# Optimization experiments

Measured on AMD Instinct MI355X. Metric: run time of the kernel, lower is better.

Reference implementation:

```python
import jax, jax.numpy as jnp
import numpy as np

HEADS = 16
GN_EPS = 1e-5
NEG = -1e30  # finite stand-in for -inf to keep softmax/vjp NaN-free


def setup_inputs() -> dict:
    key = jax.random.key(0)
    k0, k1, k2, k3 = jax.random.split(key, 4)
    B, C, T = 8, 1024, 1024
    x = jax.random.normal(k0, (B, C, T), dtype=jnp.float32)
    mask = jax.random.randint(k1, (B, T), 0, 2).astype(bool)  # True = masked position
    w_kvq = jax.random.normal(k2, (3 * C, C), dtype=jnp.float32) * 0.02  # Conv1d k=1 == per-time GEMM
    w_out = jax.random.normal(k3, (C, C), dtype=jnp.float32) * 0.02
    gn_weight = jnp.ones((C,), dtype=jnp.float32)
    gn_bias = jnp.zeros((C,), dtype=jnp.float32)
    return {"x": x, "mask": mask, "w_kvq": w_kvq, "w_out": w_out,
            "gn_weight": gn_weight, "gn_bias": gn_bias}


def reference(x, mask, w_kvq, w_out, gn_weight, gn_bias):
    B, C, T = x.shape
    H = HEADS
    d = C // H
    # QKV projection (1x1 conv == GEMM over channels)
    kvq = jnp.einsum('oc,bct->bot', w_kvq, x)  # [B, 3C, T]
    k = kvq[:, :C].reshape(B, H, d, T)
    v = kvq[:, C:2 * C].reshape(B, H, d, T)
    q = kvq[:, 2 * C:].reshape(B, H, d, T)
    scale = 1.0 / np.sqrt(d).astype(np.float32)
    # att[b,h,k,q] = <k_k, q_q> / sqrt(d)
    att = jnp.einsum('bhdk,bhdq->bhkq', k, q) * scale
    # mask key rows, softmax over key axis, then zero masked query columns
    att = jnp.where(mask[:, None, :, None], NEG, att)
    att = jax.nn.softmax(att, axis=2)
    att = jnp.where(mask[:, None, None, :], 0.0, att)
    ctx = jnp.einsum('bhdk,bhkq->bhdq', v, att).reshape(B, C, T)
    out = jnp.einsum('oc,bct->bot', w_out, ctx)
    y = out + x  # residual
    # GroupNorm(1, C): normalize over (C, T) per sample, per-channel affine
    mean = jnp.mean(y, axis=(1, 2), keepdims=True)
    var = jnp.var(y, axis=(1, 2), keepdims=True)
    y = (y - mean) * jax.lax.rsqrt(var + GN_EPS)
    y = y * gn_weight[None, :, None] + gn_bias[None, :, None]
    # torch layout of returned attention: chunks over heads concatenated on batch dim
    att_ret = att.transpose(1, 0, 2, 3).reshape(H * B, T, T)
    return y, att_ret
```

## Files before the change

kernel.cpp:

```cpp
#include <hip/hip_runtime.h>

#define DEVI __device__ __forceinline__

typedef __attribute__((ext_vector_type(8))) short s16x8;
typedef __attribute__((ext_vector_type(4))) float f32x4;
typedef __attribute__((ext_vector_type(4))) unsigned short u16x4;
typedef __attribute__((ext_vector_type(4))) int i32x4;

static constexpr int NB = 8;
static constexpr int NC = 1024;
static constexpr int NT = 1024;
static constexpr int NH = 16;
static constexpr int ND = 64;

DEVI unsigned short cvt_bf16(float f) {
  unsigned int u = __builtin_bit_cast(unsigned int, f);
  u += 0x7fffu + ((u >> 16) & 1u);
  return (unsigned short)(u >> 16);
}

DEVI float fexp2(float x) {
#if __has_builtin(__builtin_amdgcn_exp2f)
  return __builtin_amdgcn_exp2f(x);
#else
  return exp2f(x);
#endif
}

template<int ROWS>
DEVI void stage_tile(const unsigned short* g, int ld, char* lds, int loff, int tid) {
  const int wave = tid >> 6;
  const int lane = tid & 63;
#pragma unroll
  for (int r = 0; r < (ROWS >> 5); ++r) {
    const int row = r * 32 + wave * 8 + (lane >> 3);
    const int c  = lane & 7;
    const int cg = c ^ (row & 7);
    const char* src = (const char*)g + (size_t)row * ld * 2 + cg * 16;
    char* dst = lds + loff + (r * 32 + wave * 8) * 128;
    __builtin_amdgcn_global_load_lds((const __attribute__((address_space(1))) void*)src,
                                     (__attribute__((address_space(3))) void*)dst,
                                     16, 0, 0);
  }
}

DEVI void stage_v(const unsigned short* v, int k0, char* lds, int loff, int tid) {
  const int wave = tid >> 6;
  const int lane = tid & 63;
#pragma unroll
  for (int it = 0; it < 4; ++it) {
    const int d = wave * 16 + it * 4 + (lane >> 4);
    const int c = lane & 15;
    const int cg = c ^ (d & 15);
    const char* src = (const char*)(v + (size_t)d * NT + k0 + cg * 8);
    char* dst = lds + loff + (wave * 16 + it * 4) * 256;
    __builtin_amdgcn_global_load_lds((const __attribute__((address_space(1))) void*)src,
                                     (__attribute__((address_space(3))) void*)dst,
                                     16, 0, 0);
  }
}

DEVI s16x8 frag_ld(const char* lds, int loff, int row, int ks, int lane) {
  const int chunk = (ks * 4 + (lane >> 4)) ^ (row & 7);
  return *(const s16x8*)(lds + loff + row * 128 + chunk * 16);
}

template<int KTOT>
DEVI void gemm_core_128(const unsigned short* A, const unsigned short* Bt,
                        int ldA, int ldB, char* lds, int tid, f32x4 acc[4][4]) {
  const int lane = tid & 63;
  const int wave = tid >> 6;
  const int wr = wave >> 1, wc = wave & 1;
#pragma unroll
  for (int i = 0; i < 4; ++i)
#pragma unroll
    for (int j = 0; j < 4; ++j)
      acc[i][j] = (f32x4){0.f, 0.f, 0.f, 0.f};
  for (int k0 = 0; k0 < KTOT; k0 += 64) {
    __syncthreads();
    stage_tile<128>(A + k0, ldA, lds, 0, tid);
    stage_tile<128>(Bt + k0, ldB, lds, 16384, tid);
    asm volatile("s_waitcnt vmcnt(0)" ::: "memory");
    __syncthreads();
#pragma unroll
    for (int ks = 0; ks < 2; ++ks) {
      s16x8 af[4], bfr[4];
#pragma unroll
      for (int mf = 0; mf < 4; ++mf)
        af[mf] = frag_ld(lds, 0, wr * 64 + mf * 16 + (lane & 15), ks, lane);
#pragma unroll
      for (int nf = 0; nf < 4; ++nf)
        bfr[nf] = frag_ld(lds, 16384, wc * 64 + nf * 16 + (lane & 15), ks, lane);
#pragma unroll
      for (int mf = 0; mf < 4; ++mf)
#pragma unroll
        for (int nf = 0; nf < 4; ++nf)
          acc[mf][nf] = __builtin_amdgcn_mfma_f32_16x16x32_bf16(af[mf], bfr[nf], acc[mf][nf], 0, 0, 0);
    }
  }
}

__global__ __launch_bounds__(256) void k_prep(const float* __restrict__ wkvq,
                                              unsigned short* __restrict__ wkvq_bf,
                                              const float* __restrict__ wout,
                                              unsigned short* __restrict__ wout_bf) {
  const int n1 = 3 * NC * NC / 4, n2 = NC * NC / 4;
  const int stride = gridDim.x * blockDim.x;
  for (int i = blockIdx.x * blockDim.x + threadIdx.x; i < n1 + n2; i += stride) {
    const float* src = (i < n1) ? wkvq + (size_t)i * 4 : wout + (size_t)(i - n1) * 4;
    unsigned short* dst = (i < n1) ? wkvq_bf + (size_t)i * 4 : wout_bf + (size_t)(i - n1) * 4;
    f32x4 v = *(const f32x4*)src;
    u16x4 o;
#pragma unroll
    for (int j = 0; j < 4; ++j) o[j] = cvt_bf16(v[j]);
    *(u16x4*)dst = o;
  }
}

__global__ void k_xT(const float* __restrict__ x, unsigned short* __restrict__ xT) {
  __shared__ float tl[32][33];
  const int bz = blockIdx.z;
  const int t0 = blockIdx.x * 32, c0 = blockIdx.y * 32;
  const int tx = threadIdx.x, ty = threadIdx.y;
#pragma unroll
  for (int j = 0; j < 4; ++j)
    tl[ty + j * 8][tx] = x[((size_t)bz * NC + c0 + ty + j * 8) * NT + t0 + tx];
  __syncthreads();
#pragma unroll
  for (int j = 0; j < 4; ++j)
    xT[((size_t)bz * NT + t0 + ty + j * 8) * NC + c0 + tx] = cvt_bf16(tl[tx][ty + j * 8]);
}

__global__ __launch_bounds__(512, 2) void k_gemm1_256(const unsigned short* __restrict__ W,
                                                      const unsigned short* __restrict__ xT,
                                                      unsigned short* __restrict__ kt,
                                                      unsigned short* __restrict__ qt,
                                                      unsigned short* __restrict__ vbuf) {
  __shared__ char lds[131072];
  const int tid = threadIdx.x, lane = tid & 63, wid = tid >> 6;
  const int wr = wid >> 2, wc = wid & 3;
  const int gid = blockIdx.x;
  const int wg = (gid & 7) * 48 + (gid >> 3);
  const int bn = wg / 12, bm = wg % 12;

  const int r = tid >> 2, ccc = tid & 3;
  const int cg = ccc ^ ((r ^ (r >> 2)) & 3);
  const unsigned short* srcA = W + (size_t)(bm * 256 + r) * NC + cg * 8;
  const unsigned short* srcB = xT + (size_t)(bn * 256 + r) * NC + cg * 8;

  auto stageA = [&](int t) {
    char* d = lds + (t & 3) * 32768 + wid * 1024;
    const unsigned short* s = srcA + t * 32;
    __builtin_amdgcn_global_load_lds((const __attribute__((address_space(1))) void*)s,
                                     (__attribute__((address_space(3))) void*)d, 16, 0, 0);
    __builtin_amdgcn_global_load_lds((const __attribute__((address_space(1))) void*)(s + 128 * NC),
                                     (__attribute__((address_space(3))) void*)(d + 8192), 16, 0, 0);
  };
  auto stageB = [&](int t) {
    char* d = lds + (t & 3) * 32768 + 16384 + wid * 1024;
    const unsigned short* s = srcB + t * 32;
    __builtin_amdgcn_global_load_lds((const __attribute__((address_space(1))) void*)s,
                                     (__attribute__((address_space(3))) void*)d, 16, 0, 0);
    __builtin_amdgcn_global_load_lds((const __attribute__((address_space(1))) void*)(s + 128 * NC),
                                     (__attribute__((address_space(3))) void*)(d + 8192), 16, 0, 0);
  };

  const int l15 = lane & 15, lg = lane >> 4;
  const int rA = wr * 128 + l15;
  const int offA = rA * 64 + (((lg ^ (rA ^ (rA >> 2))) & 3) << 4) + ((lg & ~3) << 4);
  const int rB = wc * 64 + l15;
  const int offB = 16384 + rB * 64 + (((lg ^ (rB ^ (rB >> 2))) & 3) << 4) + ((lg & ~3) << 4);

  f32x4 acc[8][4];
#pragma unroll
  for (int i = 0; i < 8; ++i)
#pragma unroll
    for (int j = 0; j < 4; ++j) acc[i][j] = (f32x4){0.f, 0.f, 0.f, 0.f};

  stageA(0); stageB(0); stageA(1); stageB(1); stageA(2); stageB(2);
  asm volatile("s_waitcnt vmcnt(8)" ::: "memory");
  __builtin_amdgcn_s_barrier();

#pragma unroll
  for (int t = 0; t < 32; ++t) {
    const int slot = (t & 3) * 32768;
    s16x8 af[8], bf[4];
#pragma unroll
    for (int nf = 0; nf < 4; ++nf) bf[nf] = *(const s16x8*)(lds + slot + offB + nf * 1024);
#pragma unroll
    for (int mf = 0; mf < 4; ++mf) af[mf] = *(const s16x8*)(lds + slot + offA + mf * 1024);
    if (t < 29) stageA(t + 3);
    __builtin_amdgcn_s_barrier();
    asm volatile("s_waitcnt lgkmcnt(0)" ::: "memory");
    __builtin_amdgcn_sched_barrier(0);
    __builtin_amdgcn_s_setprio(1);
#pragma unroll
    for (int mf = 0; mf < 4; ++mf)
#pragma unroll
      for (int nf = 0; nf < 4; ++nf)
        acc[mf][nf] = __builtin_amdgcn_mfma_f32_16x16x32_bf16(af[mf], bf[nf], acc[mf][nf], 0, 0, 0);
    __builtin_amdgcn_s_setprio(0);
    __builtin_amdgcn_s_barrier();
#pragma unroll
    for (int mf = 4; mf < 8; ++mf) af[mf] = *(const s16x8*)(lds + slot + offA + mf * 1024);
    if (t < 29) stageB(t + 3);
    if (t < 29)       asm volatile("s_waitcnt vmcnt(8)" ::: "memory");
    else if (t == 29) asm volatile("s_waitcnt vmcnt(4)" ::: "memory");
    else              asm volatile("s_waitcnt vmcnt(0)" ::: "memory");
    __builtin_amdgcn_s_barrier();
    asm volatile("s_waitcnt lgkmcnt(0)" ::: "memory");
    __builtin_amdgcn_sched_barrier(0);
    __builtin_amdgcn_s_setprio(1);
#pragma unroll
    for (int mf = 4; mf < 8; ++mf)
#pragma unroll
      for (int nf = 0; nf < 4; ++nf)
        acc[mf][nf] = __builtin_amdgcn_mfma_f32_16x16x32_bf16(af[mf], bf[nf], acc[mf][nf], 0, 0, 0);
    __builtin_amdgcn_s_setprio(0);
    __builtin_amdgcn_s_barrier();
  }

  const int part = bm >> 2;
  const int d0base = lg << 2;
#pragma unroll
  for (int mf = 0; mf < 8; ++mf) {
    const int h = ((bm & 3) << 2) + (wr << 1) + (mf >> 2);
    const int d0 = ((mf & 3) << 4) + d0base;
#pragma unroll
    for (int nf = 0; nf < 4; ++nf) {
      const int tg = bn * 256 + wc * 64 + nf * 16 + l15;
      const int b = tg >> 10, tt = tg & 1023;
      u16x4 v4;
#pragma unroll
      for (int i = 0; i < 4; ++i) v4[i] = cvt_bf16(acc[mf][nf][i]);
      if (part == 0) {
        *(u16x4*)(kt + (((size_t)(b * NH + h) * NT + tt) * ND + d0)) = v4;
      } else if (part == 1) {
        const size_t basev = ((size_t)(b * NH + h) * ND + d0) * NT + tt;
        vbuf[basev] = v4[0]; vbuf[basev + NT] = v4[1];
        vbuf[basev + 2 * NT] = v4[2]; vbuf[basev + 3 * NT] = v4[3];
      } else {
        *(u16x4*)(qt + (((size_t)(b * NH + h) * NT + tt) * ND + d0)) = v4;
      }
    }
  }
}

__global__ __launch_bounds__(256, 2) void k_att(const unsigned short* __restrict__ kt,
                                                const unsigned short* __restrict__ qt,
                                                const unsigned short* __restrict__ vbuf,
                                                const int* __restrict__ mask,
                                                float* __restrict__ att,
                                                unsigned short* __restrict__ ctxT) {
  __shared__ char lds[81920];
  constexpr int KOFF = 0, QOFF = 16384, VOFF = 32768, POFF = 49152;
  float* colacc = (float*)(lds + POFF);
  const int tid = threadIdx.x, lane = tid & 63, wave = tid >> 6;
  const int wr = wave >> 1, wc = wave & 1;
  const int bh = blockIdx.x, qb = blockIdx.y;
  const int b = bh >> 4, h = bh & 15, hb = h * NB + b;
  const int q0 = qb * 128;
  const unsigned short* ktp = kt + (size_t)bh * NT * ND;
  const unsigned short* qtp = qt + ((size_t)bh * NT + q0) * ND;
  const unsigned short* vp  = vbuf + (size_t)bh * ND * NT;
  const int l15 = lane & 15;

  if (tid < 128) colacc[tid] = 0.f;
  stage_tile<128>(qtp, ND, lds, QOFF, tid);
  asm volatile("s_waitcnt vmcnt(0)" ::: "memory");
  __syncthreads();
  s16x8 qf[4][2];
  int qmask[4];
#pragma unroll
  for (int nf = 0; nf < 4; ++nf) {
#pragma unroll
    for (int ks = 0; ks < 2; ++ks)
      qf[nf][ks] = frag_ld(lds, QOFF, wc * 64 + nf * 16 + l15, ks, lane);
    qmask[nf] = mask[b * NT + q0 + wc * 64 + nf * 16 + l15];
  }

  const float scl = 0.125f * 1.44269504f;

  float cs[4] = {0.f, 0.f, 0.f, 0.f};
  for (int t = 0; t < 8; ++t) {
    const int k0 = t * 128;
    __syncthreads();
    stage_tile<128>(ktp + (size_t)k0 * ND, ND, lds, KOFF, tid);
    asm volatile("s_waitcnt vmcnt(0)" ::: "memory");
    __syncthreads();
    f32x4 sacc[4][4];
#pragma unroll
    for (int i = 0; i < 4; ++i)
#pragma unroll
      for (int j = 0; j < 4; ++j) sacc[i][j] = (f32x4){0.f, 0.f, 0.f, 0.f};
#pragma unroll
    for (int ks = 0; ks < 2; ++ks) {
      s16x8 kf[4];
#pragma unroll
      for (int mf = 0; mf < 4; ++mf)
        kf[mf] = frag_ld(lds, KOFF, wr * 64 + mf * 16 + l15, ks, lane);
#pragma unroll
      for (int mf = 0; mf < 4; ++mf)
#pragma unroll
        for (int nf = 0; nf < 4; ++nf)
          sacc[mf][nf] = __builtin_amdgcn_mfma_f32_16x16x32_bf16(kf[mf], qf[nf][ks], sacc[mf][nf], 0, 0, 0);
    }
#pragma unroll
    for (int mf = 0; mf < 4; ++mf) {
      const int kk0 = k0 + wr * 64 + mf * 16 + ((lane >> 4) << 2);
      const i32x4 mk = *(const i32x4*)(mask + b * NT + kk0);
#pragma unroll
      for (int nf = 0; nf < 4; ++nf)
#pragma unroll
        for (int i = 0; i < 4; ++i)
          cs[nf] += mk[i] ? 0.f : fexp2(sacc[mf][nf][i] * scl);
    }
  }
#pragma unroll
  for (int nf = 0; nf < 4; ++nf) {
    float v = cs[nf];
    v += __shfl_xor(v, 16);
    v += __shfl_xor(v, 32);
    if ((lane & 48) == 0) atomicAdd(&colacc[wc * 64 + nf * 16 + lane], v);
  }
  __syncthreads();
  float sq[4];
#pragma unroll
  for (int nf = 0; nf < 4; ++nf)
    sq[nf] = qmask[nf] ? 0.f : 1.0f / colacc[wc * 64 + nf * 16 + l15];

  f32x4 cacc[4][2];
#pragma unroll
  for (int i = 0; i < 4; ++i)
#pragma unroll
    for (int j = 0; j < 2; ++j) cacc[i][j] = (f32x4){0.f, 0.f, 0.f, 0.f};

  for (int t = 0; t < 8; ++t) {
    const int k0 = t * 128;
    __builtin_amdgcn_s_barrier();
    stage_tile<128>(ktp + (size_t)k0 * ND, ND, lds, KOFF, tid);
    stage_v(vp, k0, lds, VOFF, tid);
    asm volatile("s_waitcnt vmcnt(0)" ::: "memory");
    __builtin_amdgcn_s_barrier();

    f32x4 sacc[4][4];
#pragma unroll
    for (int i = 0; i < 4; ++i)
#pragma unroll
      for (int j = 0; j < 4; ++j) sacc[i][j] = (f32x4){0.f, 0.f, 0.f, 0.f};
#pragma unroll
    for (int ks = 0; ks < 2; ++ks) {
      s16x8 kf[4];
#pragma unroll
      for (int mf = 0; mf < 4; ++mf)
        kf[mf] = frag_ld(lds, KOFF, wr * 64 + mf * 16 + l15, ks, lane);
#pragma unroll
      for (int mf = 0; mf < 4; ++mf)
#pragma unroll
        for (int nf = 0; nf < 4; ++nf)
          sacc[mf][nf] = __builtin_amdgcn_mfma_f32_16x16x32_bf16(kf[mf], qf[nf][ks], sacc[mf][nf], 0, 0, 0);
    }

#pragma unroll
    for (int mf = 0; mf < 4; ++mf) {
      const int klocal = wr * 64 + mf * 16 + ((lane >> 4) << 2);
      const int kk0 = k0 + klocal;
      const i32x4 mk = *(const i32x4*)(mask + b * NT + kk0);
#pragma unroll
      for (int nf = 0; nf < 4; ++nf) {
        const int qloc = wc * 64 + nf * 16 + l15;
        float* ap = att + (size_t)hb * NT * NT + (size_t)kk0 * NT + q0 + qloc;
        u16x4 pb;
#pragma unroll
        for (int i = 0; i < 4; ++i) {
          const float p = mk[i] ? 0.f : fexp2(sacc[mf][nf][i] * scl) * sq[nf];
          __builtin_nontemporal_store(p, ap + (size_t)i * NT);
          pb[i] = cvt_bf16(p);
        }
        *(u16x4*)(lds + POFF + qloc * 256 + (((klocal >> 3) ^ (qloc & 15)) << 4)
                  + ((klocal & 4) << 1)) = pb;
      }
    }
    asm volatile("s_waitcnt lgkmcnt(0)" ::: "memory");
    __builtin_amdgcn_s_barrier();
    __builtin_amdgcn_sched_barrier(0);

#pragma unroll
    for (int ks2 = 0; ks2 < 4; ++ks2) {
      s16x8 vf[4], pf[2];
      const int chunk = (ks2 << 2) + (lane >> 4);
#pragma unroll
      for (int mf = 0; mf < 4; ++mf) {
        const int d = mf * 16 + l15;
        vf[mf] = *(const s16x8*)(lds + VOFF + d * 256 + ((chunk ^ (d & 15)) << 4));
      }
#pragma unroll
      for (int nf2 = 0; nf2 < 2; ++nf2) {
        const int qloc = wave * 32 + nf2 * 16 + l15;
        pf[nf2] = *(const s16x8*)(lds + POFF + qloc * 256 + ((chunk ^ (qloc & 15)) << 4));
      }
#pragma unroll
      for (int mf = 0; mf < 4; ++mf)
#pragma unroll
        for (int nf2 = 0; nf2 < 2; ++nf2)
          cacc[mf][nf2] = __builtin_amdgcn_mfma_f32_16x16x32_bf16(vf[mf], pf[nf2], cacc[mf][nf2], 0, 0, 0);
    }
  }

#pragma unroll
  for (int mf = 0; mf < 4; ++mf) {
    const int d0 = mf * 16 + ((lane >> 4) << 2);
#pragma unroll
    for (int nf2 = 0; nf2 < 2; ++nf2) {
      const int q = q0 + wave * 32 + nf2 * 16 + l15;
      u16x4 v4;
#pragma unroll
      for (int i = 0; i < 4; ++i) v4[i] = cvt_bf16(cacc[mf][nf2][i]);
      *(u16x4*)(ctxT + ((size_t)b * NT + q) * NC + h * ND + d0) = v4;
    }
  }
}

__global__ __launch_bounds__(256) void k_outgemm(const unsigned short* __restrict__ Wo,
                                                 const unsigned short* __restrict__ ctxT,
                                                 const float* __restrict__ x,
                                                 float* __restrict__ y0,
                                                 float* __restrict__ partials) {
  __shared__ char lds[32832];
  const int tid = threadIdx.x, lane = tid & 63, wave = tid >> 6;
  const int wr = wave >> 1, wc = wave & 1;
  const int bm = blockIdx.x, bn = blockIdx.y, b = blockIdx.z;
  const unsigned short* A = Wo + (size_t)bm * 128 * NC;
  const unsigned short* Bt = ctxT + ((size_t)b * NT + (size_t)bn * 128) * NC;
  f32x4 acc[4][4];
  gemm_core_128<NC>(A, Bt, NC, NC, lds, tid, acc);

  float lsum = 0.f, lsq = 0.f;
#pragma unroll
  for (int mf = 0; mf < 4; ++mf) {
#pragma unroll
    for (int nf = 0; nf < 4; ++nf) {
      const int gc = bn * 128 + wc * 64 + nf * 16 + (lane & 15);
#pragma unroll
      for (int i = 0; i < 4; ++i) {
        const int gr = bm * 128 + wr * 64 + mf * 16 + ((lane >> 4) << 2) + i;
        const size_t idx = ((size_t)b * NC + gr) * NT + gc;
        const float v = acc[mf][nf][i] + x[idx];
        y0[idx] = v;
        lsum += v; lsq += v * v;
      }
    }
  }
#pragma unroll
  for (int off = 32; off; off >>= 1) {
    lsum += __shfl_xor(lsum, off);
    lsq += __shfl_xor(lsq, off);
  }
  __syncthreads();
  float* red = (float*)(lds + 32768);
  if (lane == 0) { red[wave * 2] = lsum; red[wave * 2 + 1] = lsq; }
  __syncthreads();
  if (tid == 0) {
    const float s = red[0] + red[2] + red[4] + red[6];
    const float qq = red[1] + red[3] + red[5] + red[7];
    const int bi = bm * 8 + bn;
    partials[((size_t)b * 64 + bi) * 2] = s;
    partials[((size_t)b * 64 + bi) * 2 + 1] = qq;
  }
}

__global__ void k_gnstats(const float* __restrict__ partials, float* __restrict__ gnp) {
  const int b = blockIdx.x, t = threadIdx.x;
  float s = partials[((size_t)b * 64 + t) * 2];
  float q = partials[((size_t)b * 64 + t) * 2 + 1];
#pragma unroll
  for (int off = 32; off; off >>= 1) {
    s += __shfl_xor(s, off);
    q += __shfl_xor(q, off);
  }
  if (t == 0) {
    const float n = 1048576.f;
    const float mean = s / n;
    const float var = q / n - mean * mean;
    gnp[b * 2] = mean;
    gnp[b * 2 + 1] = rsqrtf(var + 1e-5f);
  }
}

__global__ __launch_bounds__(256) void k_gnapply(const float* __restrict__ y0,
                                                 const float* __restrict__ gnp,
                                                 const float* __restrict__ gw,
                                                 const float* __restrict__ gb,
                                                 float* __restrict__ out) {
  const size_t n4 = (size_t)NB * NC * NT / 4;
  const size_t stride = (size_t)gridDim.x * blockDim.x;
  for (size_t i = (size_t)blockIdx.x * blockDim.x + threadIdx.x; i < n4; i += stride) {
    const size_t base = i * 4;
    const int b = (int)(base >> 20);
    const int c = (int)((base >> 10) & 1023);
    const f32x4 v = *(const f32x4*)(y0 + base);
    const float m = gnp[b * 2], r = gnp[b * 2 + 1];
    const float sw = gw[c] * r, sb = gb[c];
    f32x4 o;
#pragma unroll
    for (int j = 0; j < 4; ++j) o[j] = (v[j] - m) * sw + sb;
    *(f32x4*)(out + base) = o;
  }
}

extern "C" void kernel_launch(void* const* d_in, const int* in_sizes, int n_in,
                              void* d_out, int out_size, void* d_ws, size_t ws_size,
                              hipStream_t stream) {
  (void)in_sizes; (void)n_in; (void)out_size; (void)ws_size;
  const float* x     = (const float*)d_in[0];
  const int*   mask  = (const int*)d_in[1];
  const float* w_kvq = (const float*)d_in[2];
  const float* w_out = (const float*)d_in[3];
  const float* gnw   = (const float*)d_in[4];
  const float* gnb   = (const float*)d_in[5];
  float* outy = (float*)d_out;
  float* att  = outy + (size_t)NB * NC * NT;

  char* ws = (char*)d_ws;
  unsigned short* wkvq_bf = (unsigned short*)(ws);
  unsigned short* wout_bf = (unsigned short*)(ws + 6291456);
  unsigned short* xT      = (unsigned short*)(ws + 8388608);
  unsigned short* ctxT    = xT;
  unsigned short* kt      = (unsigned short*)(ws + 25165824);
  unsigned short* qt      = (unsigned short*)(ws + 41943040);
  float*          y0      = (float*)(ws + 25165824);
  unsigned short* vbuf    = (unsigned short*)(ws + 58720256);
  float*          part    = (float*)(ws + 76021760);
  float*          gnp     = (float*)(ws + 76025856);

  k_prep<<<2048, 256, 0, stream>>>(w_kvq, wkvq_bf, w_out, wout_bf);
  k_xT<<<dim3(32, 32, 8), dim3(32, 8), 0, stream>>>(x, xT);
  k_gemm1_256<<<384, 512, 0, stream>>>(wkvq_bf, xT, kt, qt, vbuf);
  k_att<<<dim3(128, 8), 256, 0, stream>>>(kt, qt, vbuf, mask, att, ctxT);
  k_outgemm<<<dim3(8, 8, 8), 256, 0, stream>>>(wout_bf, ctxT, x, y0, part);
  k_gnstats<<<8, 64, 0, stream>>>(part, gnp);
  k_gnapply<<<4096, 256, 0, stream>>>(y0, gnp, gnw, gnb, outy);
}
```

Baseline: 347.5 us.

## Replace output GEMM with pipelined 256-tile kernel and double-buffer K in attention

Replaces the 128x128 output-projection GEMM with a 512-thread 256x256-tile kernel that uses a 4-slot LDS ring of async global-to-LDS loads, split MFMA phases with s_setprio, and an XCD-aware block remap. The GN partial layout shrinks to 16 entries per sample to match. In the attention score pass, K tiles are now double-buffered with prefetch of the next tile, and the key mask is packed into LDS bitmasks via ballot instead of being reloaded from global memory each tile. The aim is to hide load latency and cut global traffic, at the cost of 128KB of LDS per block and only 128 blocks for the output GEMM.

```diff
diff --git a/kernel.cpp b/kernel.cpp
--- a/kernel.cpp
+++ b/kernel.cpp
@@ -63,41 +63,6 @@
 DEVI s16x8 frag_ld(const char* lds, int loff, int row, int ks, int lane) {
   const int chunk = (ks * 4 + (lane >> 4)) ^ (row & 7);
   return *(const s16x8*)(lds + loff + row * 128 + chunk * 16);
-}
-
-template<int KTOT>
-DEVI void gemm_core_128(const unsigned short* A, const unsigned short* Bt,
-                        int ldA, int ldB, char* lds, int tid, f32x4 acc[4][4]) {
-  const int lane = tid & 63;
-  const int wave = tid >> 6;
-  const int wr = wave >> 1, wc = wave & 1;
-#pragma unroll
-  for (int i = 0; i < 4; ++i)
-#pragma unroll
-    for (int j = 0; j < 4; ++j)
-      acc[i][j] = (f32x4){0.f, 0.f, 0.f, 0.f};
-  for (int k0 = 0; k0 < KTOT; k0 += 64) {
-    __syncthreads();
-    stage_tile<128>(A + k0, ldA, lds, 0, tid);
-    stage_tile<128>(Bt + k0, ldB, lds, 16384, tid);
-    asm volatile("s_waitcnt vmcnt(0)" ::: "memory");
-    __syncthreads();
-#pragma unroll
-    for (int ks = 0; ks < 2; ++ks) {
-      s16x8 af[4], bfr[4];
-#pragma unroll
-      for (int mf = 0; mf < 4; ++mf)
-        af[mf] = frag_ld(lds, 0, wr * 64 + mf * 16 + (lane & 15), ks, lane);
-#pragma unroll
-      for (int nf = 0; nf < 4; ++nf)
-        bfr[nf] = frag_ld(lds, 16384, wc * 64 + nf * 16 + (lane & 15), ks, lane);
-#pragma unroll
-      for (int mf = 0; mf < 4; ++mf)
-#pragma unroll
-        for (int nf = 0; nf < 4; ++nf)
-          acc[mf][nf] = __builtin_amdgcn_mfma_f32_16x16x32_bf16(af[mf], bfr[nf], acc[mf][nf], 0, 0, 0);
-    }
-  }
 }
 
 __global__ __launch_bounds__(256) void k_prep(const float* __restrict__ wkvq,
@@ -255,6 +220,7 @@
   __shared__ char lds[81920];
   constexpr int KOFF = 0, QOFF = 16384, VOFF = 32768, POFF = 49152;
   float* colacc = (float*)(lds + POFF);
+  unsigned long long* mbits = (unsigned long long*)(lds + POFF + 512);
   const int tid = threadIdx.x, lane = tid & 63, wave = tid >> 6;
   const int wr = wave >> 1, wc = wave & 1;
   const int bh = blockIdx.x, qb = blockIdx.y;
@@ -278,16 +244,27 @@
       qf[nf][ks] = frag_ld(lds, QOFF, wc * 64 + nf * 16 + l15, ks, lane);
     qmask[nf] = mask[b * NT + q0 + wc * 64 + nf * 16 + l15];
   }
+#pragma unroll
+  for (int j = 0; j < 4; ++j) {
+    unsigned long long bb = __ballot(mask[b * NT + wave * 256 + j * 64 + lane] != 0);
+    if (lane == 0) mbits[wave * 4 + j] = bb;
+  }
+  __syncthreads();
 
   const float scl = 0.125f * 1.44269504f;
 
   float cs[4] = {0.f, 0.f, 0.f, 0.f};
+  stage_tile<128>(ktp, ND, lds, KOFF, tid);
   for (int t = 0; t < 8; ++t) {
-    const int k0 = t * 128;
-    __syncthreads();
-    stage_tile<128>(ktp + (size_t)k0 * ND, ND, lds, KOFF, tid);
-    asm volatile("s_waitcnt vmcnt(0)" ::: "memory");
-    __syncthreads();
+    __builtin_amdgcn_s_barrier();
+    if (t < 7) {
+      stage_tile<128>(ktp + (size_t)(t + 1) * 128 * ND, ND, lds, (t & 1) ? KOFF : VOFF, tid);
+      asm volatile("s_waitcnt vmcnt(4)" ::: "memory");
+    } else {
+      asm volatile("s_waitcnt vmcnt(0)" ::: "memory");
+    }
+    __builtin_amdgcn_s_barrier();
+    const int koff = (t & 1) ? VOFF : KOFF;
     f32x4 sacc[4][4];
 #pragma unroll
     for (int i = 0; i < 4; ++i)
@@ -298,7 +275,7 @@
       s16x8 kf[4];
 #pragma unroll
       for (int mf = 0; mf < 4; ++mf)
-        kf[mf] = frag_ld(lds, KOFF, wr * 64 + mf * 16 + l15, ks, lane);
+        kf[mf] = frag_ld(lds, koff, wr * 64 + mf * 16 + l15, ks, lane);
 #pragma unroll
       for (int mf = 0; mf < 4; ++mf)
 #pragma unroll
@@ -307,13 +284,13 @@
     }
 #pragma unroll
     for (int mf = 0; mf < 4; ++mf) {
-      const int kk0 = k0 + wr * 64 + mf * 16 + ((lane >> 4) << 2);
-      const i32x4 mk = *(const i32x4*)(mask + b * NT + kk0);
+      const int kk0 = t * 128 + wr * 64 + mf * 16 + ((lane >> 4) << 2);
+      const unsigned long long bw = mbits[kk0 >> 6];
 #pragma unroll
       for (int nf = 0; nf < 4; ++nf)
 #pragma unroll
         for (int i = 0; i < 4; ++i)
-          cs[nf] += mk[i] ? 0.f : fexp2(sacc[mf][nf][i] * scl);
+          cs[nf] += ((bw >> ((kk0 & 63) + i)) & 1ull) ? 0.f : fexp2(sacc[mf][nf][i] * scl);
     }
   }
 #pragma unroll
@@ -421,32 +398,108 @@
   }
 }
 
-__global__ __launch_bounds__(256) void k_outgemm(const unsigned short* __restrict__ Wo,
-                                                 const unsigned short* __restrict__ ctxT,
-                                                 const float* __restrict__ x,
-                                                 float* __restrict__ y0,
-                                                 float* __restrict__ partials) {
-  __shared__ char lds[32832];
-  const int tid = threadIdx.x, lane = tid & 63, wave = tid >> 6;
-  const int wr = wave >> 1, wc = wave & 1;
-  const int bm = blockIdx.x, bn = blockIdx.y, b = blockIdx.z;
-  const unsigned short* A = Wo + (size_t)bm * 128 * NC;
-  const unsigned short* Bt = ctxT + ((size_t)b * NT + (size_t)bn * 128) * NC;
-  f32x4 acc[4][4];
-  gemm_core_128<NC>(A, Bt, NC, NC, lds, tid, acc);
-
+__global__ __launch_bounds__(512, 2) void k_outgemm_256(const unsigned short* __restrict__ Wo,
+                                                        const unsigned short* __restrict__ ctxT,
+                                                        const float* __restrict__ x,
+                                                        float* __restrict__ y0,
+                                                        float* __restrict__ partials) {
+  __shared__ char lds[131072];
+  const int tid = threadIdx.x, lane = tid & 63, wid = tid >> 6;
+  const int wr = wid >> 2, wc = wid & 3;
+  const int gid = blockIdx.x;
+  const int wg = (gid & 7) * 16 + (gid >> 3);
+  const int bm = wg & 3, bn = wg >> 2;
+
+  const int r = tid >> 2, ccc = tid & 3;
+  const int cg = ccc ^ ((r ^ (r >> 2)) & 3);
+  const unsigned short* srcA = Wo + (size_t)(bm * 256 + r) * NC + cg * 8;
+  const unsigned short* srcB = ctxT + (size_t)(bn * 256 + r) * NC + cg * 8;
+
+  auto stageA = [&](int t) {
+    char* d = lds + (t & 3) * 32768 + wid * 1024;
+    const unsigned short* s = srcA + t * 32;
+    __builtin_amdgcn_global_load_lds((const __attribute__((address_space(1))) void*)s,
+                                     (__attribute__((address_space(3))) void*)d, 16, 0, 0);
+    __builtin_amdgcn_global_load_lds((const __attribute__((address_space(1))) void*)(s + 128 * NC),
+                                     (__attribute__((address_space(3))) void*)(d + 8192), 16, 0, 0);
+  };
+  auto stageB = [&](int t) {
+    char* d = lds + (t & 3) * 32768 + 16384 + wid * 1024;
+    const unsigned short* s = srcB + t * 32;
+    __builtin_amdgcn_global_load_lds((const __attribute__((address_space(1))) void*)s,
+                                     (__attribute__((address_space(3))) void*)d, 16, 0, 0);
+    __builtin_amdgcn_global_load_lds((const __attribute__((address_space(1))) void*)(s + 128 * NC),
+                                     (__attribute__((address_space(3))) void*)(d + 8192), 16, 0, 0);
+  };
+
+  const int l15 = lane & 15, lg = lane >> 4;
+  const int rA = wr * 128 + l15;
+  const int offA = rA * 64 + (((lg ^ (rA ^ (rA >> 2))) & 3) << 4) + ((lg & ~3) << 4);
+  const int rB = wc * 64 + l15;
+  const int offB = 16384 + rB * 64 + (((lg ^ (rB ^ (rB >> 2))) & 3) << 4) + ((lg & ~3) << 4);
+
+  f32x4 acc[8][4];
+#pragma unroll
+  for (int i = 0; i < 8; ++i)
+#pragma unroll
+    for (int j = 0; j < 4; ++j) acc[i][j] = (f32x4){0.f, 0.f, 0.f, 0.f};
+
+  stageA(0); stageB(0); stageA(1); stageB(1); stageA(2); stageB(2);
+  asm volatile("s_waitcnt vmcnt(8)" ::: "memory");
+  __builtin_amdgcn_s_barrier();
+
+#pragma unroll
+  for (int t = 0; t < 32; ++t) {
+    const int slot = (t & 3) * 32768;
+    s16x8 af[8], bf[4];
+#pragma unroll
+    for (int nf = 0; nf < 4; ++nf) bf[nf] = *(const s16x8*)(lds + slot + offB + nf * 1024);
+#pragma unroll
+    for (int mf = 0; mf < 4; ++mf) af[mf] = *(const s16x8*)(lds + slot + offA + mf * 1024);
+    if (t < 29) stageA(t + 3);
+    __builtin_amdgcn_s_barrier();
+    asm volatile("s_waitcnt lgkmcnt(0)" ::: "memory");
+    __builtin_amdgcn_sched_barrier(0);
+    __builtin_amdgcn_s_setprio(1);
+#pragma unroll
+    for (int mf = 0; mf < 4; ++mf)
+#pragma unroll
+      for (int nf = 0; nf < 4; ++nf)
+        acc[mf][nf] = __builtin_amdgcn_mfma_f32_16x16x32_bf16(af[mf], bf[nf], acc[mf][nf], 0, 0, 0);
+    __builtin_amdgcn_s_setprio(0);
+    __builtin_amdgcn_s_barrier();
+#pragma unroll
+    for (int mf = 4; mf < 8; ++mf) af[mf] = *(const s16x8*)(lds + slot + offA + mf * 1024);
+    if (t < 29) stageB(t + 3);
+    if (t < 29)       asm volatile("s_waitcnt vmcnt(8)" ::: "memory");
+    else if (t == 29) asm volatile("s_waitcnt vmcnt(4)" ::: "memory");
+    else              asm volatile("s_waitcnt vmcnt(0)" ::: "memory");
+    __builtin_amdgcn_s_barrier();
+    asm volatile("s_waitcnt lgkmcnt(0)" ::: "memory");
+    __builtin_amdgcn_sched_barrier(0);
+    __builtin_amdgcn_s_setprio(1);
+#pragma unroll
+    for (int mf = 4; mf < 8; ++mf)
+#pragma unroll
+      for (int nf = 0; nf < 4; ++nf)
+        acc[mf][nf] = __builtin_amdgcn_mfma_f32_16x16x32_bf16(af[mf], bf[nf], acc[mf][nf], 0, 0, 0);
+    __builtin_amdgcn_s_setprio(0);
+    __builtin_amdgcn_s_barrier();
+  }
+
+  const int b = bn >> 2;
   float lsum = 0.f, lsq = 0.f;
 #pragma unroll
-  for (int mf = 0; mf < 4; ++mf) {
+  for (int mf = 0; mf < 8; ++mf) {
+    const int c = bm * 256 + wr * 128 + mf * 16 + (lg << 2);
 #pragma unroll
     for (int nf = 0; nf < 4; ++nf) {
-      const int gc = bn * 128 + wc * 64 + nf * 16 + (lane & 15);
+      const int tt = ((bn & 3) << 8) + wc * 64 + nf * 16 + l15;
+      const size_t idx = ((size_t)b * NC + c) * NT + tt;
 #pragma unroll
       for (int i = 0; i < 4; ++i) {
-        const int gr = bm * 128 + wr * 64 + mf * 16 + ((lane >> 4) << 2) + i;
-        const size_t idx = ((size_t)b * NC + gr) * NT + gc;
-        const float v = acc[mf][nf][i] + x[idx];
-        y0[idx] = v;
+        const float v = acc[mf][nf][i] + x[idx + (size_t)i * NT];
+        y0[idx + (size_t)i * NT] = v;
         lsum += v; lsq += v * v;
       }
     }
@@ -457,24 +510,28 @@
     lsq += __shfl_xor(lsq, off);
   }
   __syncthreads();
-  float* red = (float*)(lds + 32768);
-  if (lane == 0) { red[wave * 2] = lsum; red[wave * 2 + 1] = lsq; }
+  float* red = (float*)lds;
+  if (lane == 0) { red[wid * 2] = lsum; red[wid * 2 + 1] = lsq; }
   __syncthreads();
   if (tid == 0) {
-    const float s = red[0] + red[2] + red[4] + red[6];
-    const float qq = red[1] + red[3] + red[5] + red[7];
-    const int bi = bm * 8 + bn;
-    partials[((size_t)b * 64 + bi) * 2] = s;
-    partials[((size_t)b * 64 + bi) * 2 + 1] = qq;
+    float s = 0.f, qq = 0.f;
+#pragma unroll
+    for (int j = 0; j < 8; ++j) { s += red[j * 2]; qq += red[j * 2 + 1]; }
+    const int slot = ((bn & 3) << 2) + bm;
+    partials[((size_t)b * 16 + slot) * 2] = s;
+    partials[((size_t)b * 16 + slot) * 2 + 1] = qq;
   }
 }
 
 __global__ void k_gnstats(const float* __restrict__ partials, float* __restrict__ gnp) {
   const int b = blockIdx.x, t = threadIdx.x;
-  float s = partials[((size_t)b * 64 + t) * 2];
-  float q = partials[((size_t)b * 64 + t) * 2 + 1];
-#pragma unroll
-  for (int off = 32; off; off >>= 1) {
+  float s = 0.f, q = 0.f;
+  if (t < 16) {
+    s = partials[((size_t)b * 16 + t) * 2];
+    q = partials[((size_t)b * 16 + t) * 2 + 1];
+  }
+#pragma unroll
+  for (int off = 8; off; off >>= 1) {
     s += __shfl_xor(s, off);
     q += __shfl_xor(q, off);
   }
@@ -537,7 +594,7 @@
   k_xT<<<dim3(32, 32, 8), dim3(32, 8), 0, stream>>>(x, xT);
   k_gemm1_256<<<384, 512, 0, stream>>>(wkvq_bf, xT, kt, qt, vbuf);
   k_att<<<dim3(128, 8), 256, 0, stream>>>(kt, qt, vbuf, mask, att, ctxT);
-  k_outgemm<<<dim3(8, 8, 8), 256, 0, stream>>>(wout_bf, ctxT, x, y0, part);
+  k_outgemm_256<<<128, 512, 0, stream>>>(wout_bf, ctxT, x, y0, part);
   k_gnstats<<<8, 64, 0, stream>>>(part, gnp);
   k_gnapply<<<4096, 256, 0, stream>>>(y0, gnp, gnw, gnb, outy);
 }
```

Result: no change. 354.3 us (+2.0%).

## Double-buffer K tiles, prefetch K/V across phases, vectorize att stores, bitmask key masks

Applied to the files above, without the earlier changes.

The first (column-sum) pass now double-buffers K tiles in LDS, using the V region as the second buffer, so the next tile's load overlaps the current MFMA work. The second pass issues the next K and V tile loads early and uses partial vmcnt waits. MFMA operands are swapped so each lane holds four consecutive query columns, which allows 16-byte nontemporal stores of the attention matrix instead of scalar ones. Key masks are packed into per-lane bitmasks via ballot instead of being reloaded from global memory each tile. In exchange, the bf16 P writes to LDS become scalar 2-byte stores, and correctness depends on the hand-counted vmcnt values and the extra barriers.

```diff
diff --git a/kernel.cpp b/kernel.cpp
--- a/kernel.cpp
+++ b/kernel.cpp
@@ -255,6 +255,7 @@
   __shared__ char lds[81920];
   constexpr int KOFF = 0, QOFF = 16384, VOFF = 32768, POFF = 49152;
   float* colacc = (float*)(lds + POFF);
+  unsigned long long* mbits = (unsigned long long*)(lds + POFF + 512);
   const int tid = threadIdx.x, lane = tid & 63, wave = tid >> 6;
   const int wr = wave >> 1, wc = wave & 1;
   const int bh = blockIdx.x, qb = blockIdx.y;
@@ -263,31 +264,54 @@
   const unsigned short* ktp = kt + (size_t)bh * NT * ND;
   const unsigned short* qtp = qt + ((size_t)bh * NT + q0) * ND;
   const unsigned short* vp  = vbuf + (size_t)bh * ND * NT;
-  const int l15 = lane & 15;
+  const int l15 = lane & 15, g = lane >> 4;
 
   if (tid < 128) colacc[tid] = 0.f;
   stage_tile<128>(qtp, ND, lds, QOFF, tid);
+#pragma unroll
+  for (int j = 0; j < 4; ++j) {
+    unsigned long long bb = __ballot(mask[b * NT + wave * 256 + j * 64 + lane] != 0);
+    if (lane == 0) mbits[wave * 4 + j] = bb;
+  }
+  i32x4 qm4[4];
+#pragma unroll
+  for (int nf = 0; nf < 4; ++nf)
+    qm4[nf] = *(const i32x4*)(mask + b * NT + q0 + wc * 64 + nf * 16 + g * 4);
   asm volatile("s_waitcnt vmcnt(0)" ::: "memory");
   __syncthreads();
+
   s16x8 qf[4][2];
-  int qmask[4];
-#pragma unroll
-  for (int nf = 0; nf < 4; ++nf) {
+#pragma unroll
+  for (int nf = 0; nf < 4; ++nf)
 #pragma unroll
     for (int ks = 0; ks < 2; ++ks)
       qf[nf][ks] = frag_ld(lds, QOFF, wc * 64 + nf * 16 + l15, ks, lane);
-    qmask[nf] = mask[b * NT + q0 + wc * 64 + nf * 16 + l15];
+
+  unsigned int kmask32 = 0;
+#pragma unroll
+  for (int t = 0; t < 8; ++t) {
+    const unsigned long long w64 = mbits[t * 2 + wr];
+#pragma unroll
+    for (int mf = 0; mf < 4; ++mf)
+      kmask32 |= (unsigned int)((w64 >> (mf * 16 + l15)) & 1ull) << (t * 4 + mf);
   }
 
   const float scl = 0.125f * 1.44269504f;
 
-  float cs[4] = {0.f, 0.f, 0.f, 0.f};
+  f32x4 cs4[4];
+#pragma unroll
+  for (int nf = 0; nf < 4; ++nf) cs4[nf] = (f32x4){0.f, 0.f, 0.f, 0.f};
+  stage_tile<128>(ktp, ND, lds, KOFF, tid);
   for (int t = 0; t < 8; ++t) {
-    const int k0 = t * 128;
-    __syncthreads();
-    stage_tile<128>(ktp + (size_t)k0 * ND, ND, lds, KOFF, tid);
-    asm volatile("s_waitcnt vmcnt(0)" ::: "memory");
-    __syncthreads();
+    __builtin_amdgcn_s_barrier();
+    if (t < 7) {
+      stage_tile<128>(ktp + (size_t)(t + 1) * 128 * ND, ND, lds, (t & 1) ? KOFF : VOFF, tid);
+      asm volatile("s_waitcnt vmcnt(4)" ::: "memory");
+    } else {
+      asm volatile("s_waitcnt vmcnt(0)" ::: "memory");
+    }
+    __builtin_amdgcn_s_barrier();
+    const int koff = (t & 1) ? VOFF : KOFF;
     f32x4 sacc[4][4];
 #pragma unroll
     for (int i = 0; i < 4; ++i)
@@ -298,36 +322,46 @@
       s16x8 kf[4];
 #pragma unroll
       for (int mf = 0; mf < 4; ++mf)
-        kf[mf] = frag_ld(lds, KOFF, wr * 64 + mf * 16 + l15, ks, lane);
+        kf[mf] = frag_ld(lds, koff, wr * 64 + mf * 16 + l15, ks, lane);
 #pragma unroll
       for (int mf = 0; mf < 4; ++mf)
 #pragma unroll
         for (int nf = 0; nf < 4; ++nf)
-          sacc[mf][nf] = __builtin_amdgcn_mfma_f32_16x16x32_bf16(kf[mf], qf[nf][ks], sacc[mf][nf], 0, 0, 0);
+          sacc[mf][nf] = __builtin_amdgcn_mfma_f32_16x16x32_bf16(qf[nf][ks], kf[mf], sacc[mf][nf], 0, 0, 0);
     }
 #pragma unroll
     for (int mf = 0; mf < 4; ++mf) {
-      const int kk0 = k0 + wr * 64 + mf * 16 + ((lane >> 4) << 2);
-      const i32x4 mk = *(const i32x4*)(mask + b * NT + kk0);
+      const float kz = ((kmask32 >> (t * 4 + mf)) & 1u) ? 0.f : 1.f;
 #pragma unroll
       for (int nf = 0; nf < 4; ++nf)
 #pragma unroll
         for (int i = 0; i < 4; ++i)
-          cs[nf] += mk[i] ? 0.f : fexp2(sacc[mf][nf][i] * scl);
-    }
-  }
-#pragma unroll
-  for (int nf = 0; nf < 4; ++nf) {
-    float v = cs[nf];
-    v += __shfl_xor(v, 16);
-    v += __shfl_xor(v, 32);
-    if ((lane & 48) == 0) atomicAdd(&colacc[wc * 64 + nf * 16 + lane], v);
+          cs4[nf][i] += kz * fexp2(sacc[mf][nf][i] * scl);
+    }
+  }
+#pragma unroll
+  for (int nf = 0; nf < 4; ++nf)
+#pragma unroll
+    for (int i = 0; i < 4; ++i) {
+      float v = cs4[nf][i];
+      v += __shfl_xor(v, 1); v += __shfl_xor(v, 2);
+      v += __shfl_xor(v, 4); v += __shfl_xor(v, 8);
+      cs4[nf][i] = v;
+    }
+  if (l15 == 0) {
+#pragma unroll
+    for (int nf = 0; nf < 4; ++nf)
+#pragma unroll
+      for (int i = 0; i < 4; ++i)
+        atomicAdd(&colacc[wc * 64 + nf * 16 + g * 4 + i], cs4[nf][i]);
   }
   __syncthreads();
-  float sq[4];
+  f32x4 sq4[4];
 #pragma unroll
   for (int nf = 0; nf < 4; ++nf)
-    sq[nf] = qmask[nf] ? 0.f : 1.0f / colacc[wc * 64 + nf * 16 + l15];
+#pragma unroll
+    for (int i = 0; i < 4; ++i)
+      sq4[nf][i] = qm4[nf][i] ? 0.f : 1.0f / colacc[wc * 64 + nf * 16 + g * 4 + i];
 
   f32x4 cacc[4][2];
 #pragma unroll
@@ -335,14 +369,13 @@
 #pragma unroll
     for (int j = 0; j < 2; ++j) cacc[i][j] = (f32x4){0.f, 0.f, 0.f, 0.f};
 
+  stage_tile<128>(ktp, ND, lds, KOFF, tid);
+  stage_v(vp, 0, lds, VOFF, tid);
+  asm volatile("s_waitcnt vmcnt(0)" ::: "memory");
+  __builtin_amdgcn_s_barrier();
+
+  float* attb = att + (size_t)hb * NT * NT + q0 + wc * 64 + g * 4;
   for (int t = 0; t < 8; ++t) {
-    const int k0 = t * 128;
-    __builtin_amdgcn_s_barrier();
-    stage_tile<128>(ktp + (size_t)k0 * ND, ND, lds, KOFF, tid);
-    stage_v(vp, k0, lds, VOFF, tid);
-    asm volatile("s_waitcnt vmcnt(0)" ::: "memory");
-    __builtin_amdgcn_s_barrier();
-
     f32x4 sacc[4][4];
 #pragma unroll
     for (int i = 0; i < 4; ++i)
@@ -358,37 +391,45 @@
       for (int mf = 0; mf < 4; ++mf)
 #pragma unroll
         for (int nf = 0; nf < 4; ++nf)
-          sacc[mf][nf] = __builtin_amdgcn_mfma_f32_16x16x32_bf16(kf[mf], qf[nf][ks], sacc[mf][nf], 0, 0, 0);
-    }
+          sacc[mf][nf] = __builtin_amdgcn_mfma_f32_16x16x32_bf16(qf[nf][ks], kf[mf], sacc[mf][nf], 0, 0, 0);
+    }
+    __builtin_amdgcn_s_barrier();
+    if (t < 7) stage_tile<128>(ktp + (size_t)(t + 1) * 128 * ND, ND, lds, KOFF, tid);
+    __builtin_amdgcn_sched_barrier(0);
 
 #pragma unroll
     for (int mf = 0; mf < 4; ++mf) {
-      const int klocal = wr * 64 + mf * 16 + ((lane >> 4) << 2);
-      const int kk0 = k0 + klocal;
-      const i32x4 mk = *(const i32x4*)(mask + b * NT + kk0);
+      const int kg = t * 128 + wr * 64 + mf * 16 + l15;
+      const float kz = ((kmask32 >> (t * 4 + mf)) & 1u) ? 0.f : 1.f;
+      const int kloc = wr * 64 + mf * 16 + l15;
 #pragma unroll
       for (int nf = 0; nf < 4; ++nf) {
-        const int qloc = wc * 64 + nf * 16 + l15;
-        float* ap = att + (size_t)hb * NT * NT + (size_t)kk0 * NT + q0 + qloc;
-        u16x4 pb;
+        f32x4 p4;
+#pragma unroll
+        for (int i = 0; i < 4; ++i)
+          p4[i] = kz * fexp2(sacc[mf][nf][i] * scl) * sq4[nf][i];
+        __builtin_nontemporal_store(p4, (f32x4*)(attb + (size_t)kg * NT + nf * 16));
+        const int qrow = wc * 64 + nf * 16 + g * 4;
 #pragma unroll
         for (int i = 0; i < 4; ++i) {
-          const float p = mk[i] ? 0.f : fexp2(sacc[mf][nf][i] * scl) * sq[nf];
-          __builtin_nontemporal_store(p, ap + (size_t)i * NT);
-          pb[i] = cvt_bf16(p);
+          const int row = qrow + i;
+          *(unsigned short*)(lds + POFF + row * 256 + (((kloc >> 3) ^ (row & 15)) << 4)
+                             + ((kloc & 7) << 1)) = cvt_bf16(p4[i]);
         }
-        *(u16x4*)(lds + POFF + qloc * 256 + (((klocal >> 3) ^ (qloc & 15)) << 4)
-                  + ((klocal & 4) << 1)) = pb;
       }
     }
     asm volatile("s_waitcnt lgkmcnt(0)" ::: "memory");
-    __builtin_amdgcn_s_barrier();
     __builtin_amdgcn_sched_barrier(0);
+    __builtin_amdgcn_s_barrier();
+    if (t > 0) {
+      if (t < 7) asm volatile("s_waitcnt vmcnt(20)" ::: "memory");
+      else       asm volatile("s_waitcnt vmcnt(16)" ::: "memory");
+    }
 
 #pragma unroll
     for (int ks2 = 0; ks2 < 4; ++ks2) {
       s16x8 vf[4], pf[2];
-      const int chunk = (ks2 << 2) + (lane >> 4);
+      const int chunk = (ks2 << 2) + g;
 #pragma unroll
       for (int mf = 0; mf < 4; ++mf) {
         const int d = mf * 16 + l15;
@@ -405,11 +446,17 @@
         for (int nf2 = 0; nf2 < 2; ++nf2)
           cacc[mf][nf2] = __builtin_amdgcn_mfma_f32_16x16x32_bf16(vf[mf], pf[nf2], cacc[mf][nf2], 0, 0, 0);
     }
+    __builtin_amdgcn_s_barrier();
+    if (t < 7) {
+      stage_v(vp, (t + 1) * 128, lds, VOFF, tid);
+      asm volatile("s_waitcnt vmcnt(20)" ::: "memory");
+      __builtin_amdgcn_s_barrier();
+    }
   }
 
 #pragma unroll
   for (int mf = 0; mf < 4; ++mf) {
-    const int d0 = mf * 16 + ((lane >> 4) << 2);
+    const int d0 = mf * 16 + (g << 2);
 #pragma unroll
     for (int nf2 = 0; nf2 < 2; ++nf2) {
       const int q = q0 + wave * 32 + nf2 * 16 + l15;
```

Measured after the change: 346.6 us. About the same (-0.3%).
